# Kernel tuning notes

Measured on AMD Instinct MI355X. Metric: run time of the kernel, lower is better.

Reference implementation:

```python
import jax, jax.numpy as jnp
import numpy as np

I = 16    # nutrition_input_size
H = 128   # hidden_size
B = 64
S = 4096
MLP = 64


def setup_inputs() -> dict:
    key = jax.random.key(0)
    ks = jax.random.split(key, 16)
    sc = 0.05
    inp = {
        "nutrition_data": jax.random.normal(ks[0], (B, S, I), dtype=jnp.float32),
        # GRU layer 0 (input size I)
        "w_ih0": sc * jax.random.normal(ks[1], (3 * H, I), dtype=jnp.float32),
        "w_hh0": sc * jax.random.normal(ks[2], (3 * H, H), dtype=jnp.float32),
        "b_ih0": sc * jax.random.normal(ks[3], (3 * H,), dtype=jnp.float32),
        "b_hh0": sc * jax.random.normal(ks[4], (3 * H,), dtype=jnp.float32),
        # GRU layer 1 (input size H)
        "w_ih1": sc * jax.random.normal(ks[5], (3 * H, H), dtype=jnp.float32),
        "w_hh1": sc * jax.random.normal(ks[6], (3 * H, H), dtype=jnp.float32),
        "b_ih1": sc * jax.random.normal(ks[7], (3 * H,), dtype=jnp.float32),
        "b_hh1": sc * jax.random.normal(ks[8], (3 * H,), dtype=jnp.float32),
        # metabolism increment head: Linear(H+I, 64) -> ReLU -> Linear(64, 1)
        "w1": sc * jax.random.normal(ks[9], (MLP, H + I), dtype=jnp.float32),
        "b1": sc * jax.random.normal(ks[10], (MLP,), dtype=jnp.float32),
        "w2": sc * jax.random.normal(ks[11], (1, MLP), dtype=jnp.float32),
        "b2": sc * jax.random.normal(ks[12], (1,), dtype=jnp.float32),
        "initial_metabolism": jnp.float32(2.5),
    }
    return inp


def _gru_layer(x, w_ih, w_hh, b_ih, b_hh):
    # x: [B, S, D]; PyTorch GRU cell math, gate order (r, z, n).
    gi = jnp.einsum("bsd,gd->bsg", x, w_ih) + b_ih  # [B, S, 3H]
    h0 = jnp.zeros((x.shape[0], w_hh.shape[1]), dtype=x.dtype)

    def step(h, gi_t):
        gh = h @ w_hh.T + b_hh  # [B, 3H]
        i_r, i_z, i_n = jnp.split(gi_t, 3, axis=-1)
        h_r, h_z, h_n = jnp.split(gh, 3, axis=-1)
        r = jax.nn.sigmoid(i_r + h_r)
        z = jax.nn.sigmoid(i_z + h_z)
        n = jnp.tanh(i_n + r * h_n)
        h_new = (1.0 - z) * n + z * h
        return h_new, h_new

    _, hs = jax.lax.scan(step, h0, jnp.swapaxes(gi, 0, 1))  # hs: [S, B, H]
    return jnp.swapaxes(hs, 0, 1)  # [B, S, H]


def reference(nutrition_data, w_ih0, w_hh0, b_ih0, b_hh0,
              w_ih1, w_hh1, b_ih1, b_hh1,
              w1, b1, w2, b2, initial_metabolism):
    # 2-layer GRU (dropout is inactive in eval; identical math without it)
    h1 = _gru_layer(nutrition_data, w_ih0, w_hh0, b_ih0, b_hh0)
    gru_out = _gru_layer(h1, w_ih1, w_hh1, b_ih1, b_hh1)  # [B, S, H]

    # Per-timestep head is independent of recurrence: batch it over all t,
    # then replace the sequential additive accumulation with a cumsum.
    combined = jnp.concatenate([gru_out, nutrition_data], axis=-1)  # [B, S, H+I]
    hdn = jax.nn.relu(jnp.einsum("bsf,mf->bsm", combined, w1) + b1)
    inc = jnp.tanh(jnp.einsum("bsm,om->bso", hdn, w2) + b2) * 0.125  # [B, S, 1]
    out = initial_metabolism + jnp.cumsum(inc, axis=1)  # [B, S, 1]
    return out
```

## Files before the change

### kernel.cpp

```cpp
#include <hip/hip_runtime.h>
#include <cmath>

#define B 64
#define S 4096
#define NI 16
#define H 128
#define F 144
#define CH 16
#define NCH (S / CH)

typedef _Float16 h2   __attribute__((ext_vector_type(2)));
typedef _Float16 h4v  __attribute__((ext_vector_type(4)));
typedef _Float16 h8   __attribute__((ext_vector_type(8)));
typedef float    f4v  __attribute__((ext_vector_type(4)));
typedef unsigned long long u64;
typedef u64 u64x2 __attribute__((ext_vector_type(2)));

__device__ __forceinline__ float rcp_fast(float x) { return __builtin_amdgcn_rcpf(x); }
__device__ __forceinline__ float sigf(float x) {
    return rcp_fast(1.0f + __expf(-x));
}
__device__ __forceinline__ float tanh_fast(float x) {
    const float e = __expf(-2.0f * x);
    return fmaf(2.0f, rcp_fast(1.0f + e), -1.0f);
}
__device__ __forceinline__ float quad_reduce(float v) {
    int t1 = __builtin_amdgcn_mov_dpp(__float_as_int(v), 0xB1, 0xf, 0xf, true);
    v += __int_as_float(t1);
    int t2 = __builtin_amdgcn_mov_dpp(__float_as_int(v), 0x4E, 0xf, 0xf, true);
    v += __int_as_float(t2);
    return v;
}
__device__ __forceinline__ float pair_reduce(float v) {
    int t1 = __builtin_amdgcn_mov_dpp(__float_as_int(v), 0xB1, 0xf, 0xf, true);
    v += __int_as_float(t1);
    return v;
}
__device__ __forceinline__ h2 cvt2(float a, float b) {
    h2 r; r[0] = (_Float16)a; r[1] = (_Float16)b; return r;
}
__device__ __forceinline__ void cvt8(const float* p, h2* w) {
    const float4 f0 = ((const float4*)p)[0];
    const float4 f1 = ((const float4*)p)[1];
    w[0] = cvt2(f0.x, f0.y); w[1] = cvt2(f0.z, f0.w);
    w[2] = cvt2(f1.x, f1.y); w[3] = cvt2(f1.z, f1.w);
}
__device__ __forceinline__ h8 cvt8v(const float* p) {
    const float4 f0 = ((const float4*)p)[0];
    const float4 f1 = ((const float4*)p)[1];
    h8 r;
    r[0] = (_Float16)f0.x; r[1] = (_Float16)f0.y;
    r[2] = (_Float16)f0.z; r[3] = (_Float16)f0.w;
    r[4] = (_Float16)f1.x; r[5] = (_Float16)f1.y;
    r[6] = (_Float16)f1.z; r[7] = (_Float16)f1.w;
    return r;
}
__device__ __forceinline__ void pin_h2(h2& v) {
    int t = __builtin_bit_cast(int, v);
    asm volatile("" : "+v"(t));
    v = __builtin_bit_cast(h2, t);
}
__device__ __forceinline__ void pin_f(float& v) {
    asm volatile("" : "+v"(v));
}
__device__ __forceinline__ void pin_h8(h8& v) {
    u64x2 t = __builtin_bit_cast(u64x2, v);
    u64 a = t[0], b = t[1];
    asm volatile("" : "+v"(a), "+v"(b));
    t[0] = a; t[1] = b;
    v = __builtin_bit_cast(h8, t);
}
__device__ __forceinline__ f4v mfma16(h8 a, h8 b, f4v c) {
    return __builtin_amdgcn_mfma_f32_16x16x32_f16(a, b, c, 0, 0, 0);
}

__device__ __forceinline__ void store_y0(void* p, uint2 v) {
    __hip_atomic_store((u64*)p, __builtin_bit_cast(u64, v),
                       __ATOMIC_RELAXED, __HIP_MEMORY_SCOPE_AGENT);
}
__device__ __forceinline__ h8 load_y0_h8(const _Float16* p) {
    u64x2 v;
    v[0] = __hip_atomic_load((const u64*)p,     __ATOMIC_RELAXED, __HIP_MEMORY_SCOPE_AGENT);
    v[1] = __hip_atomic_load((const u64*)p + 1, __ATOMIC_RELAXED, __HIP_MEMORY_SCOPE_AGENT);
    return __builtin_bit_cast(h8, v);
}
__device__ __forceinline__ void wait_flag(int* f) {
    int spins = 0;
    while (__hip_atomic_load(f, __ATOMIC_ACQUIRE, __HIP_MEMORY_SCOPE_AGENT) == 0) {
        __builtin_amdgcn_s_sleep(8);
        if (++spins > (1 << 17)) break;
    }
}
__device__ __forceinline__ void post_flag(int* f) {
    __hip_atomic_store(f, 1, __ATOMIC_RELEASE, __HIP_MEMORY_SCOPE_AGENT);
}

__global__ __launch_bounds__(512, 2)
void gru_pipe(const float* __restrict__ x,
              const float* __restrict__ w_ih0, const float* __restrict__ w_hh0,
              const float* __restrict__ b_ih0, const float* __restrict__ b_hh0,
              const float* __restrict__ w_ih1, const float* __restrict__ w_hh1,
              const float* __restrict__ b_ih1, const float* __restrict__ b_hh1,
              _Float16* __restrict__ hbuf, int* __restrict__ flags)
{
    const int tid = threadIdx.x;
    const int b = blockIdx.x >> 1;
    const bool producer = (blockIdx.x & 1) == 0;

    if (producer) {
        const int j = tid >> 2;
        const int m = tid & 3;

        __shared__ __align__(16) _Float16 sH0[2][H];
        __shared__ __align__(16) _Float16 sX[2][CH][NI];
        __shared__ __align__(16) _Float16 sYo[2][CH][H];

        h2 wh[48];
        h2 wx[6];
#pragma unroll
        for (int g = 0; g < 3; g++) {
            const float* wr = w_hh0 + (size_t)(g * H + j) * H;
#pragma unroll
            for (int i = 0; i < 4; i++) {
                const int f = (i + m) & 3;
                cvt8(wr + 32 * m + 8 * f, &wh[g * 16 + 4 * i]);
            }
            const float4 wv = *(const float4*)(w_ih0 + (size_t)(g * H + j) * NI + 4 * m);
            wx[g * 2 + 0] = cvt2(wv.x, wv.y);
            wx[g * 2 + 1] = cvt2(wv.z, wv.w);
        }
        float b_r  = b_ih0[j]       + b_hh0[j];
        float b_z  = b_ih0[H + j]   + b_hh0[H + j];
        float b_in = b_ih0[2*H + j];
        float b_hn = b_hh0[2*H + j];
#pragma unroll
        for (int i = 0; i < 48; i++) pin_h2(wh[i]);
#pragma unroll
        for (int i = 0; i < 6; i++) pin_h2(wx[i]);
        pin_f(b_r); pin_f(b_z); pin_f(b_in); pin_f(b_hn);

        const float* xb = x + (size_t)b * S * NI;
        _Float16*    yb = hbuf + (size_t)b * S * H;
        int*         fb = flags + b * NCH;

        float4 xreg = {0.f, 0.f, 0.f, 0.f};
        if (tid < H) sH0[0][tid] = (_Float16)0.0f;
        if (tid < 64) {
            const float4 v = ((const float4*)xb)[tid];
            h4v p; p[0] = (_Float16)v.x; p[1] = (_Float16)v.y;
                   p[2] = (_Float16)v.z; p[3] = (_Float16)v.w;
            ((h4v*)&sX[0][0][0])[tid] = p;
            xreg = ((const float4*)(xb + CH * NI))[tid];
        }
        float hprev = 0.0f;
        __syncthreads();

        for (int k = 0; k <= S; k++) {
            const int cur = k & 1;
            const int c0  = k >> 4;
            const int tw  = k & (CH - 1);

            if (tw == 0 && k >= CH) {
                const int cp = c0 - 1;
                const uint2 v = ((const uint2*)&sYo[cp & 1][0][0])[tid];
                store_y0((char*)(yb + (size_t)cp * CH * H) + 8 * tid, v);
            }
            if (tw == 1 && k >= CH + 1 && tid == 0) post_flag(fb + (c0 - 1));

            if (k < S) {
                if (tw == 0 && tid < 64) {
                    const int cn = c0 + 1;
                    if (cn < NCH) {
                        h4v p; p[0] = (_Float16)xreg.x; p[1] = (_Float16)xreg.y;
                               p[2] = (_Float16)xreg.z; p[3] = (_Float16)xreg.w;
                        ((h4v*)&sX[cn & 1][0][0])[tid] = p;
                        if (cn + 1 < NCH)
                            xreg = ((const float4*)(xb + (size_t)(cn + 1) * CH * NI))[tid];
                    }
                }

                const float4* hv = (const float4*)&sH0[cur][0];
                float ar = 0.f, az = 0.f, ahn = 0.f;
#pragma unroll
                for (int i = 0; i < 4; i++) {
                    const int f = (i + m) & 3;
                    const float4 q = hv[4 * m + f];
                    const h2 p0 = __builtin_bit_cast(h2, q.x);
                    const h2 p1 = __builtin_bit_cast(h2, q.y);
                    const h2 p2 = __builtin_bit_cast(h2, q.z);
                    const h2 p3 = __builtin_bit_cast(h2, q.w);
                    ar  = __builtin_amdgcn_fdot2(p0, wh[4*i+0],    ar,  false);
                    ar  = __builtin_amdgcn_fdot2(p1, wh[4*i+1],    ar,  false);
                    ar  = __builtin_amdgcn_fdot2(p2, wh[4*i+2],    ar,  false);
                    ar  = __builtin_amdgcn_fdot2(p3, wh[4*i+3],    ar,  false);
                    az  = __builtin_amdgcn_fdot2(p0, wh[16+4*i+0], az,  false);
                    az  = __builtin_amdgcn_fdot2(p1, wh[16+4*i+1], az,  false);
                    az  = __builtin_amdgcn_fdot2(p2, wh[16+4*i+2], az,  false);
                    az  = __builtin_amdgcn_fdot2(p3, wh[16+4*i+3], az,  false);
                    ahn = __builtin_amdgcn_fdot2(p0, wh[32+4*i+0], ahn, false);
                    ahn = __builtin_amdgcn_fdot2(p1, wh[32+4*i+1], ahn, false);
                    ahn = __builtin_amdgcn_fdot2(p2, wh[32+4*i+2], ahn, false);
                    ahn = __builtin_amdgcn_fdot2(p3, wh[32+4*i+3], ahn, false);
                }
                const float2 xq = *(const float2*)&sX[c0 & 1][tw][4 * m];
                const h2 x0 = __builtin_bit_cast(h2, xq.x);
                const h2 x1 = __builtin_bit_cast(h2, xq.y);
                float ain = 0.f;
                ar  = __builtin_amdgcn_fdot2(x0, wx[0], ar,  false);
                ar  = __builtin_amdgcn_fdot2(x1, wx[1], ar,  false);
                az  = __builtin_amdgcn_fdot2(x0, wx[2], az,  false);
                az  = __builtin_amdgcn_fdot2(x1, wx[3], az,  false);
                ain = __builtin_amdgcn_fdot2(x0, wx[4], ain, false);
                ain = __builtin_amdgcn_fdot2(x1, wx[5], ain, false);

                const float vr  = quad_reduce(ar)  + b_r;
                const float vz  = quad_reduce(az)  + b_z;
                const float vin = quad_reduce(ain) + b_in;
                const float vhn = quad_reduce(ahn) + b_hn;

                const float r  = sigf(vr);
                const float z  = sigf(vz);
                const float n  = tanh_fast(vin + r * vhn);
                const float hn = n + z * (hprev - n);
                hprev = hn;
                if (m == 0) {
                    sH0[cur ^ 1][j]     = (_Float16)hn;
                    sYo[c0 & 1][tw][j]  = (_Float16)hn;
                }
            }
            __syncthreads();
        }
        if (tid == 0) post_flag(fb + (NCH - 1));
    } else {
        __shared__ __align__(16) _Float16 sH1[2][H];
        __shared__ __align__(16) float    sGi[2][CH][3][H];
        __shared__ __align__(16) _Float16 sHo[2][CH][H];

        _Float16* yb = hbuf + (size_t)b * S * H;
        int*      fb = flags + b * NCH;

        const bool isRec = (tid < 256);
        const int lane = tid & 63;
        const int jr = (tid & 255) >> 1;
        const int mr = tid & 1;
        const int wv = (tid >> 6) - 4;
        const int nl = lane & 15;
        const int q  = lane >> 4;

        h2 wc[96];
        float b_hn = 0.0f;
        h8 Bf[6][4];
        float bias[6];
        h8 Apre[4];

        if (isRec) {
#pragma unroll
            for (int g = 0; g < 3; g++) {
#pragma unroll
                for (int i = 0; i < 8; i++) {
                    const int ii = (i + 4 * mr) & 7;
                    cvt8(w_hh1 + (size_t)(g * H + jr) * H + 64 * mr + 8 * ii,
                         &wc[g * 32 + 4 * i]);
                }
            }
            b_hn = b_hh1[2 * H + jr];
#pragma unroll
            for (int i = 0; i < 96; i++) pin_h2(wc[i]);
            pin_f(b_hn);
            if (tid < H) sH1[0][tid] = (_Float16)0.0f;
        } else {
#pragma unroll
            for (int tt = 0; tt < 6; tt++) {
                const int n = 16 * (wv * 6 + tt) + nl;
                const float* wr = w_ih1 + (size_t)n * H;
#pragma unroll
                for (int kc = 0; kc < 4; kc++)
                    Bf[tt][kc] = cvt8v(wr + 32 * kc + 8 * q);
                bias[tt] = b_ih1[n] + (n < 2 * H ? b_hh1[n] : 0.0f);
            }
#pragma unroll
            for (int tt = 0; tt < 6; tt++) {
#pragma unroll
                for (int kc = 0; kc < 4; kc++) pin_h8(Bf[tt][kc]);
                pin_f(bias[tt]);
            }
            if (lane == 0) wait_flag(fb + 0);
            {
                const _Float16* yrow = yb + (size_t)nl * H;
                h8 A0c[4];
#pragma unroll
                for (int kc = 0; kc < 4; kc++)
                    A0c[kc] = load_y0_h8(yrow + 32 * kc + 8 * q);
                f4v a0 = {0.f,0.f,0.f,0.f}, a1 = a0, a2 = a0, a3 = a0, a4 = a0, a5 = a0;
#pragma unroll
                for (int kc = 0; kc < 4; kc++) {
                    a0 = mfma16(A0c[kc], Bf[0][kc], a0);
                    a1 = mfma16(A0c[kc], Bf[1][kc], a1);
                    a2 = mfma16(A0c[kc], Bf[2][kc], a2);
                    a3 = mfma16(A0c[kc], Bf[3][kc], a3);
                    a4 = mfma16(A0c[kc], Bf[4][kc], a4);
                    a5 = mfma16(A0c[kc], Bf[5][kc], a5);
                }
                f4v accs[6] = {a0, a1, a2, a3, a4, a5};
                float* gp = &sGi[0][0][0][0];
#pragma unroll
                for (int tt = 0; tt < 6; tt++) {
                    const int n = 16 * (wv * 6 + tt) + nl;
                    const int g = n >> 7, jj = n & 127;
#pragma unroll
                    for (int r = 0; r < 4; r++)
                        gp[((4 * q + r) * 3 + g) * H + jj] = accs[tt][r] + bias[tt];
                }
            }
        }
        float hprev = 0.0f;
        __syncthreads();

        for (int t = 0; t < S; t++) {
            const int cur = t & 1;
            const int c   = t >> 4;
            const int tw  = t & (CH - 1);

            if (isRec) {
                const float gr = sGi[c & 1][tw][0][jr];
                const float gz = sGi[c & 1][tw][1][jr];
                const float gn = sGi[c & 1][tw][2][jr];
                const float4* hv = (const float4*)&sH1[cur][0];
                float ar = 0.f, az = 0.f, ahn = 0.f;
#pragma unroll
                for (int i = 0; i < 8; i++) {
                    const int ii = (i + 4 * mr) & 7;
                    const float4 qv = hv[8 * mr + ii];
                    const h2 p0 = __builtin_bit_cast(h2, qv.x);
                    const h2 p1 = __builtin_bit_cast(h2, qv.y);
                    const h2 p2 = __builtin_bit_cast(h2, qv.z);
                    const h2 p3 = __builtin_bit_cast(h2, qv.w);
                    ar  = __builtin_amdgcn_fdot2(p0, wc[4*i+0],      ar,  false);
                    ar  = __builtin_amdgcn_fdot2(p1, wc[4*i+1],      ar,  false);
                    ar  = __builtin_amdgcn_fdot2(p2, wc[4*i+2],      ar,  false);
                    ar  = __builtin_amdgcn_fdot2(p3, wc[4*i+3],      ar,  false);
                    az  = __builtin_amdgcn_fdot2(p0, wc[32+4*i+0],   az,  false);
                    az  = __builtin_amdgcn_fdot2(p1, wc[32+4*i+1],   az,  false);
                    az  = __builtin_amdgcn_fdot2(p2, wc[32+4*i+2],   az,  false);
                    az  = __builtin_amdgcn_fdot2(p3, wc[32+4*i+3],   az,  false);
                    ahn = __builtin_amdgcn_fdot2(p0, wc[64+4*i+0],   ahn, false);
                    ahn = __builtin_amdgcn_fdot2(p1, wc[64+4*i+1],   ahn, false);
                    ahn = __builtin_amdgcn_fdot2(p2, wc[64+4*i+2],   ahn, false);
                    ahn = __builtin_amdgcn_fdot2(p3, wc[64+4*i+3],   ahn, false);
                }
                const float r  = sigf(pair_reduce(ar) + gr);
                const float z  = sigf(pair_reduce(az) + gz);
                const float n  = tanh_fast(gn + r * (pair_reduce(ahn) + b_hn));
                const float hn = n + z * (hprev - n);
                hprev = hn;
                if (mr == 0) {
                    sH1[cur ^ 1][jr]   = (_Float16)hn;
                    sHo[c & 1][tw][jr] = (_Float16)hn;
                }
            } else {
                if (tw == 0) {
                    if (c >= 1) {
                        const int cp  = c - 1;
                        const int idx = tid - 256;
                        const uint2 v0 = ((const uint2*)&sHo[cp & 1][0][0])[idx];
                        const uint2 v1 = ((const uint2*)&sHo[cp & 1][0][0])[idx + 256];
                        ((uint2*)(yb + (size_t)cp * CH * H))[idx]       = v0;
                        ((uint2*)(yb + (size_t)cp * CH * H))[idx + 256] = v1;
                    }
                    if (c + 1 < NCH) {
                        if (lane == 0) wait_flag(fb + (c + 1));
                        const _Float16* yrow = yb + ((size_t)(c + 1) * CH + nl) * H;
#pragma unroll
                        for (int kc = 0; kc < 4; kc++)
                            Apre[kc] = load_y0_h8(yrow + 32 * kc + 8 * q);
                    }
                } else if (tw == 1 && c + 1 < NCH) {
                    f4v a0 = {0.f,0.f,0.f,0.f}, a1 = a0, a2 = a0, a3 = a0, a4 = a0, a5 = a0;
#pragma unroll
                    for (int kc = 0; kc < 4; kc++) {
                        a0 = mfma16(Apre[kc], Bf[0][kc], a0);
                        a1 = mfma16(Apre[kc], Bf[1][kc], a1);
                        a2 = mfma16(Apre[kc], Bf[2][kc], a2);
                        a3 = mfma16(Apre[kc], Bf[3][kc], a3);
                        a4 = mfma16(Apre[kc], Bf[4][kc], a4);
                        a5 = mfma16(Apre[kc], Bf[5][kc], a5);
                    }
                    f4v accs[6] = {a0, a1, a2, a3, a4, a5};
                    float* gp = &sGi[(c + 1) & 1][0][0][0];
#pragma unroll
                    for (int tt = 0; tt < 6; tt++) {
                        const int n = 16 * (wv * 6 + tt) + nl;
                        const int g = n >> 7, jj = n & 127;
#pragma unroll
                        for (int r = 0; r < 4; r++)
                            gp[((4 * q + r) * 3 + g) * H + jj] = accs[tt][r] + bias[tt];
                    }
                }
            }
            __syncthreads();
        }
        if (!isRec) {
            const int cp  = NCH - 1;
            const int idx = tid - 256;
            const uint2 v0 = ((const uint2*)&sHo[cp & 1][0][0])[idx];
            const uint2 v1 = ((const uint2*)&sHo[cp & 1][0][0])[idx + 256];
            ((uint2*)(yb + (size_t)cp * CH * H))[idx]       = v0;
            ((uint2*)(yb + (size_t)cp * CH * H))[idx + 256] = v1;
        }
    }
}

__global__ __launch_bounds__(256, 2)
void head_mfma(const _Float16* __restrict__ h1, const float* __restrict__ x,
               const float* __restrict__ w1, const float* __restrict__ b1,
               const float* __restrict__ w2, const float* __restrict__ b2,
               float* __restrict__ inc)
{
    const int wave = threadIdx.x >> 6;
    const int lane = threadIdx.x & 63;
    const int nl   = lane & 15;
    const int q    = lane >> 4;

    h8 Bf[4][5];
    float b1v[4], w2v[4];
#pragma unroll
    for (int t = 0; t < 4; t++) {
        const int n = 16 * t + nl;
        const float* wr = w1 + (size_t)n * F;
#pragma unroll
        for (int c = 0; c < 4; c++)
            Bf[t][c] = cvt8v(wr + 32 * c + 8 * q);
        if (q < 2) Bf[t][4] = cvt8v(wr + 128 + 8 * q);
        else { h8 z = {};
               Bf[t][4] = z; }
        b1v[t] = b1[n];
        w2v[t] = w2[n];
    }
    const float b2v = b2[0];

    const int gw = blockIdx.x * 4 + wave;

    for (int it = 0; it < 8; it++) {
        const int row0 = (gw * 8 + it) * 16;
        const int rm   = row0 + nl;

        const _Float16* hp = h1 + (size_t)rm * H;
        h8 A0 = *(const h8*)(hp + 8 * q);
        h8 A1 = *(const h8*)(hp + 32 + 8 * q);
        h8 A2 = *(const h8*)(hp + 64 + 8 * q);
        h8 A3 = *(const h8*)(hp + 96 + 8 * q);
        h8 A4;
        if (q < 2) A4 = cvt8v(x + (size_t)rm * NI + 8 * q);
        else { h8 z = {}; A4 = z; }

        f4v acc0 = {0.f,0.f,0.f,0.f}, acc1 = {0.f,0.f,0.f,0.f};
        f4v acc2 = {0.f,0.f,0.f,0.f}, acc3 = {0.f,0.f,0.f,0.f};
        acc0 = mfma16(A0, Bf[0][0], acc0); acc1 = mfma16(A0, Bf[1][0], acc1);
        acc2 = mfma16(A0, Bf[2][0], acc2); acc3 = mfma16(A0, Bf[3][0], acc3);
        acc0 = mfma16(A1, Bf[0][1], acc0); acc1 = mfma16(A1, Bf[1][1], acc1);
        acc2 = mfma16(A1, Bf[2][1], acc2); acc3 = mfma16(A1, Bf[3][1], acc3);
        acc0 = mfma16(A2, Bf[0][2], acc0); acc1 = mfma16(A2, Bf[1][2], acc1);
        acc2 = mfma16(A2, Bf[2][2], acc2); acc3 = mfma16(A2, Bf[3][2], acc3);
        acc0 = mfma16(A3, Bf[0][3], acc0); acc1 = mfma16(A3, Bf[1][3], acc1);
        acc2 = mfma16(A3, Bf[2][3], acc2); acc3 = mfma16(A3, Bf[3][3], acc3);
        acc0 = mfma16(A4, Bf[0][4], acc0); acc1 = mfma16(A4, Bf[1][4], acc1);
        acc2 = mfma16(A4, Bf[2][4], acc2); acc3 = mfma16(A4, Bf[3][4], acc3);

        float rs[4];
#pragma unroll
        for (int r = 0; r < 4; r++) {
            rs[r] = fmaxf(acc0[r] + b1v[0], 0.f) * w2v[0]
                  + fmaxf(acc1[r] + b1v[1], 0.f) * w2v[1]
                  + fmaxf(acc2[r] + b1v[2], 0.f) * w2v[2]
                  + fmaxf(acc3[r] + b1v[3], 0.f) * w2v[3];
        }
#pragma unroll
        for (int off = 1; off < 16; off <<= 1) {
#pragma unroll
            for (int r = 0; r < 4; r++)
                rs[r] += __shfl_xor(rs[r], off, 64);
        }
        if (nl == 0) {
            float4 o;
            o.x = tanh_fast(rs[0] + b2v) * 0.125f;
            o.y = tanh_fast(rs[1] + b2v) * 0.125f;
            o.z = tanh_fast(rs[2] + b2v) * 0.125f;
            o.w = tanh_fast(rs[3] + b2v) * 0.125f;
            *(float4*)(inc + row0 + 4 * q) = o;
        }
    }
}

__global__ __launch_bounds__(256)
void cumsum_kernel(const float* __restrict__ inc, const float* __restrict__ init,
                   float* __restrict__ out)
{
    __shared__ float sW[4];
    const int b = blockIdx.x;
    const int tid = threadIdx.x;
    const int lane = tid & 63;
    const int wid = tid >> 6;

    const float* ib = inc + (size_t)b * S;
    float v[16];
#pragma unroll
    for (int i = 0; i < 16; i++) v[i] = ib[tid * 16 + i];

    float run = 0.f;
#pragma unroll
    for (int i = 0; i < 16; i++) { run += v[i]; v[i] = run; }

    float t = run;
#pragma unroll
    for (int off = 1; off < 64; off <<= 1) {
        float u = __shfl_up(t, off, 64);
        if (lane >= off) t += u;
    }
    const float excl = t - run;
    if (lane == 63) sW[wid] = t;
    __syncthreads();

    float wo = 0.f;
#pragma unroll
    for (int w = 0; w < 4; w++) if (w < wid) wo += sW[w];

    const float prefix = wo + excl + init[0];
    float* ob = out + (size_t)b * S;
#pragma unroll
    for (int i = 0; i < 16; i++) ob[tid * 16 + i] = prefix + v[i];
}

extern "C" void kernel_launch(void* const* d_in, const int* in_sizes, int n_in,
                              void* d_out, int out_size, void* d_ws, size_t ws_size,
                              hipStream_t stream)
{
    (void)in_sizes; (void)n_in; (void)out_size; (void)ws_size;
    const float* x     = (const float*)d_in[0];
    const float* w_ih0 = (const float*)d_in[1];
    const float* w_hh0 = (const float*)d_in[2];
    const float* b_ih0 = (const float*)d_in[3];
    const float* b_hh0 = (const float*)d_in[4];
    const float* w_ih1 = (const float*)d_in[5];
    const float* w_hh1 = (const float*)d_in[6];
    const float* b_ih1 = (const float*)d_in[7];
    const float* b_hh1 = (const float*)d_in[8];
    const float* w1    = (const float*)d_in[9];
    const float* b1    = (const float*)d_in[10];
    const float* w2    = (const float*)d_in[11];
    const float* b2    = (const float*)d_in[12];
    const float* init  = (const float*)d_in[13];
    float* out = (float*)d_out;

    _Float16* hbuf = (_Float16*)d_ws;
    float* incbuf  = (float*)((char*)d_ws + (size_t)B * S * H * 2);
    int* flags     = (int*)((char*)d_ws + (size_t)B * S * H * 2
                                        + (size_t)B * S * 4);

    hipMemsetAsync(flags, 0, (size_t)B * NCH * sizeof(int), stream);

    hipLaunchKernelGGL(gru_pipe, dim3(2 * B), dim3(512), 0, stream,
                       x, w_ih0, w_hh0, b_ih0, b_hh0,
                       w_ih1, w_hh1, b_ih1, b_hh1, hbuf, flags);
    hipLaunchKernelGGL(head_mfma, dim3(512), dim3(256), 0, stream,
                       hbuf, x, w1, b1, w2, b2, incbuf);
    hipLaunchKernelGGL(cumsum_kernel, dim3(B), dim3(256), 0, stream,
                       incbuf, init, out);
}
```

Before: 2.511 ms.

## Unify producer and consumer GRU blocks with MFMA input projection for layer 0

```diff
diff --git a/kernel.cpp b/kernel.cpp
--- a/kernel.cpp
+++ b/kernel.cpp
@@ -8,9 +8,9 @@
 #define F 144
 #define CH 16
 #define NCH (S / CH)
+#define GIP 201
 
 typedef _Float16 h2   __attribute__((ext_vector_type(2)));
-typedef _Float16 h4v  __attribute__((ext_vector_type(4)));
 typedef _Float16 h8   __attribute__((ext_vector_type(8)));
 typedef float    f4v  __attribute__((ext_vector_type(4)));
 typedef unsigned long long u64;
@@ -23,13 +23,6 @@
 __device__ __forceinline__ float tanh_fast(float x) {
     const float e = __expf(-2.0f * x);
     return fmaf(2.0f, rcp_fast(1.0f + e), -1.0f);
-}
-__device__ __forceinline__ float quad_reduce(float v) {
-    int t1 = __builtin_amdgcn_mov_dpp(__float_as_int(v), 0xB1, 0xf, 0xf, true);
-    v += __int_as_float(t1);
-    int t2 = __builtin_amdgcn_mov_dpp(__float_as_int(v), 0x4E, 0xf, 0xf, true);
-    v += __int_as_float(t2);
-    return v;
 }
 __device__ __forceinline__ float pair_reduce(float v) {
     int t1 = __builtin_amdgcn_mov_dpp(__float_as_int(v), 0xB1, 0xf, 0xf, true);
@@ -95,7 +88,19 @@
     __hip_atomic_store(f, 1, __ATOMIC_RELEASE, __HIP_MEMORY_SCOPE_AGENT);
 }
 
-__global__ __launch_bounds__(512, 2)
+__device__ __forceinline__ void write_gi(float* gp, const f4v* accs,
+                                         const float* bias, int wv, int nl, int q) {
+#pragma unroll
+    for (int tt = 0; tt < 6; tt++) {
+        const int n = 16 * (wv * 6 + tt) + nl;
+        const int g = n >> 7, jj = n & 127;
+#pragma unroll
+        for (int r = 0; r < 4; r++)
+            gp[((4 * q + r) * 3 + g) * GIP + jj] = accs[tt][r] + bias[tt];
+    }
+}
+
+__global__ __launch_bounds__(512, 1)
 void gru_pipe(const float* __restrict__ x,
               const float* __restrict__ w_ih0, const float* __restrict__ w_hh0,
               const float* __restrict__ b_ih0, const float* __restrict__ b_hh0,
@@ -103,311 +108,204 @@
               const float* __restrict__ b_ih1, const float* __restrict__ b_hh1,
               _Float16* __restrict__ hbuf, int* __restrict__ flags)
 {
+    __shared__ __align__(16) _Float16 sH[2][H];
+    __shared__ __align__(16) float    sGi[2][CH][3][GIP];
+    __shared__ __align__(16) _Float16 sO[2][CH][H];
+
     const int tid = threadIdx.x;
     const int b = blockIdx.x >> 1;
     const bool producer = (blockIdx.x & 1) == 0;
-
-    if (producer) {
-        const int j = tid >> 2;
-        const int m = tid & 3;
-
-        __shared__ __align__(16) _Float16 sH0[2][H];
-        __shared__ __align__(16) _Float16 sX[2][CH][NI];
-        __shared__ __align__(16) _Float16 sYo[2][CH][H];
-
-        h2 wh[48];
-        h2 wx[6];
-#pragma unroll
-        for (int g = 0; g < 3; g++) {
-            const float* wr = w_hh0 + (size_t)(g * H + j) * H;
-#pragma unroll
-            for (int i = 0; i < 4; i++) {
-                const int f = (i + m) & 3;
-                cvt8(wr + 32 * m + 8 * f, &wh[g * 16 + 4 * i]);
+    const bool isRec = tid < 256;
+    const int lane = tid & 63;
+    const int jr = (tid & 255) >> 1;
+    const int mr = tid & 1;
+    const int wv = (tid >> 6) - 4;
+    const int nl = lane & 15;
+    const int q  = lane >> 4;
+
+    const float* xb = x + (size_t)b * S * NI;
+    _Float16*    yb = hbuf + (size_t)b * S * H;
+    int*         fb = flags + b * NCH;
+
+    h2 wc[96];
+    float b_hn = 0.0f;
+    h8 Bf[6][4];
+    float bias[6];
+    h8 Apre[4];
+
+    if (isRec) {
+        const float* whh = producer ? w_hh0 : w_hh1;
+        const float* bhh = producer ? b_hh0 : b_hh1;
+#pragma unroll
+        for (int g = 0; g < 3; g++)
+#pragma unroll
+            for (int i = 0; i < 8; i++) {
+                const int ii = (i + 4 * mr) & 7;
+                cvt8(whh + (size_t)(g * H + jr) * H + 64 * mr + 8 * ii,
+                     &wc[g * 32 + 4 * i]);
             }
-            const float4 wv = *(const float4*)(w_ih0 + (size_t)(g * H + j) * NI + 4 * m);
-            wx[g * 2 + 0] = cvt2(wv.x, wv.y);
-            wx[g * 2 + 1] = cvt2(wv.z, wv.w);
-        }
-        float b_r  = b_ih0[j]       + b_hh0[j];
-        float b_z  = b_ih0[H + j]   + b_hh0[H + j];
-        float b_in = b_ih0[2*H + j];
-        float b_hn = b_hh0[2*H + j];
-#pragma unroll
-        for (int i = 0; i < 48; i++) pin_h2(wh[i]);
-#pragma unroll
-        for (int i = 0; i < 6; i++) pin_h2(wx[i]);
-        pin_f(b_r); pin_f(b_z); pin_f(b_in); pin_f(b_hn);
-
-        const float* xb = x + (size_t)b * S * NI;
-        _Float16*    yb = hbuf + (size_t)b * S * H;
-        int*         fb = flags + b * NCH;
-
-        float4 xreg = {0.f, 0.f, 0.f, 0.f};
-        if (tid < H) sH0[0][tid] = (_Float16)0.0f;
-        if (tid < 64) {
-            const float4 v = ((const float4*)xb)[tid];
-            h4v p; p[0] = (_Float16)v.x; p[1] = (_Float16)v.y;
-                   p[2] = (_Float16)v.z; p[3] = (_Float16)v.w;
-            ((h4v*)&sX[0][0][0])[tid] = p;
-            xreg = ((const float4*)(xb + CH * NI))[tid];
-        }
-        float hprev = 0.0f;
-        __syncthreads();
-
-        for (int k = 0; k <= S; k++) {
-            const int cur = k & 1;
-            const int c0  = k >> 4;
-            const int tw  = k & (CH - 1);
-
-            if (tw == 0 && k >= CH) {
-                const int cp = c0 - 1;
-                const uint2 v = ((const uint2*)&sYo[cp & 1][0][0])[tid];
-                store_y0((char*)(yb + (size_t)cp * CH * H) + 8 * tid, v);
+        b_hn = bhh[2 * H + jr];
+#pragma unroll
+        for (int i = 0; i < 96; i++) pin_h2(wc[i]);
+        pin_f(b_hn);
+        if (tid < H) sH[0][tid] = (_Float16)0.0f;
+    } else if (producer) {
+#pragma unroll
+        for (int tt = 0; tt < 6; tt++) {
+            const int n = 16 * (wv * 6 + tt) + nl;
+            if (q < 2) Bf[tt][0] = cvt8v(w_ih0 + (size_t)n * NI + 8 * q);
+            else { h8 z = {}; Bf[tt][0] = z; }
+            bias[tt] = b_ih0[n] + (n < 2 * H ? b_hh0[n] : 0.0f);
+            pin_h8(Bf[tt][0]); pin_f(bias[tt]);
+        }
+        h8 A;
+        if (q < 2) A = cvt8v(xb + (size_t)nl * NI + 8 * q);
+        else { h8 z = {}; A = z; }
+        f4v accs[6];
+#pragma unroll
+        for (int tt = 0; tt < 6; tt++) {
+            f4v zz = {0.f, 0.f, 0.f, 0.f};
+            accs[tt] = mfma16(A, Bf[tt][0], zz);
+        }
+        write_gi(&sGi[0][0][0][0], accs, bias, wv, nl, q);
+    } else {
+#pragma unroll
+        for (int tt = 0; tt < 6; tt++) {
+            const int n = 16 * (wv * 6 + tt) + nl;
+            const float* wr = w_ih1 + (size_t)n * H;
+#pragma unroll
+            for (int kc = 0; kc < 4; kc++) {
+                Bf[tt][kc] = cvt8v(wr + 32 * kc + 8 * q);
+                pin_h8(Bf[tt][kc]);
             }
-            if (tw == 1 && k >= CH + 1 && tid == 0) post_flag(fb + (c0 - 1));
-
-            if (k < S) {
-                if (tw == 0 && tid < 64) {
-                    const int cn = c0 + 1;
-                    if (cn < NCH) {
-                        h4v p; p[0] = (_Float16)xreg.x; p[1] = (_Float16)xreg.y;
-                               p[2] = (_Float16)xreg.z; p[3] = (_Float16)xreg.w;
-                        ((h4v*)&sX[cn & 1][0][0])[tid] = p;
-                        if (cn + 1 < NCH)
-                            xreg = ((const float4*)(xb + (size_t)(cn + 1) * CH * NI))[tid];
-                    }
-                }
-
-                const float4* hv = (const float4*)&sH0[cur][0];
-                float ar = 0.f, az = 0.f, ahn = 0.f;
-#pragma unroll
-                for (int i = 0; i < 4; i++) {
-                    const int f = (i + m) & 3;
-                    const float4 q = hv[4 * m + f];
-                    const h2 p0 = __builtin_bit_cast(h2, q.x);
-                    const h2 p1 = __builtin_bit_cast(h2, q.y);
-                    const h2 p2 = __builtin_bit_cast(h2, q.z);
-                    const h2 p3 = __builtin_bit_cast(h2, q.w);
-                    ar  = __builtin_amdgcn_fdot2(p0, wh[4*i+0],    ar,  false);
-                    ar  = __builtin_amdgcn_fdot2(p1, wh[4*i+1],    ar,  false);
-                    ar  = __builtin_amdgcn_fdot2(p2, wh[4*i+2],    ar,  false);
-                    ar  = __builtin_amdgcn_fdot2(p3, wh[4*i+3],    ar,  false);
-                    az  = __builtin_amdgcn_fdot2(p0, wh[16+4*i+0], az,  false);
-                    az  = __builtin_amdgcn_fdot2(p1, wh[16+4*i+1], az,  false);
-                    az  = __builtin_amdgcn_fdot2(p2, wh[16+4*i+2], az,  false);
-                    az  = __builtin_amdgcn_fdot2(p3, wh[16+4*i+3], az,  false);
-                    ahn = __builtin_amdgcn_fdot2(p0, wh[32+4*i+0], ahn, false);
-                    ahn = __builtin_amdgcn_fdot2(p1, wh[32+4*i+1], ahn, false);
-                    ahn = __builtin_amdgcn_fdot2(p2, wh[32+4*i+2], ahn, false);
-                    ahn = __builtin_amdgcn_fdot2(p3, wh[32+4*i+3], ahn, false);
-                }
-                const float2 xq = *(const float2*)&sX[c0 & 1][tw][4 * m];
-                const h2 x0 = __builtin_bit_cast(h2, xq.x);
-                const h2 x1 = __builtin_bit_cast(h2, xq.y);
-                float ain = 0.f;
-                ar  = __builtin_amdgcn_fdot2(x0, wx[0], ar,  false);
-                ar  = __builtin_amdgcn_fdot2(x1, wx[1], ar,  false);
-                az  = __builtin_amdgcn_fdot2(x0, wx[2], az,  false);
-                az  = __builtin_amdgcn_fdot2(x1, wx[3], az,  false);
-                ain = __builtin_amdgcn_fdot2(x0, wx[4], ain, false);
-                ain = __builtin_amdgcn_fdot2(x1, wx[5], ain, false);
-
-                const float vr  = quad_reduce(ar)  + b_r;
-                const float vz  = quad_reduce(az)  + b_z;
-                const float vin = quad_reduce(ain) + b_in;
-                const float vhn = quad_reduce(ahn) + b_hn;
-
-                const float r  = sigf(vr);
-                const float z  = sigf(vz);
-                const float n  = tanh_fast(vin + r * vhn);
-                const float hn = n + z * (hprev - n);
-                hprev = hn;
-                if (m == 0) {
-                    sH0[cur ^ 1][j]     = (_Float16)hn;
-                    sYo[c0 & 1][tw][j]  = (_Float16)hn;
-                }
+            bias[tt] = b_ih1[n] + (n < 2 * H ? b_hh1[n] : 0.0f);
+            pin_f(bias[tt]);
+        }
+        if (lane == 0) wait_flag(fb + 0);
+        const _Float16* yrow = yb + (size_t)nl * H;
+        h8 A0c[4];
+#pragma unroll
+        for (int kc = 0; kc < 4; kc++)
+            A0c[kc] = load_y0_h8(yrow + 32 * kc + 8 * q);
+        f4v accs[6];
+#pragma unroll
+        for (int tt = 0; tt < 6; tt++) { f4v zz = {0.f,0.f,0.f,0.f}; accs[tt] = zz; }
+#pragma unroll
+        for (int kc = 0; kc < 4; kc++)
+#pragma unroll
+            for (int tt = 0; tt < 6; tt++)
+                accs[tt] = mfma16(A0c[kc], Bf[tt][kc], accs[tt]);
+        write_gi(&sGi[0][0][0][0], accs, bias, wv, nl, q);
+    }
+    float hprev = 0.0f;
+    __syncthreads();
+
+    for (int t = 0; t < S; t++) {
+        const int cur = t & 1;
+        const int c   = t >> 4;
+        const int tw  = t & (CH - 1);
+
+        if (isRec) {
+            const float gr = sGi[c & 1][tw][0][jr];
+            const float gz = sGi[c & 1][tw][1][jr];
+            const float gn = sGi[c & 1][tw][2][jr];
+            const float4* hv = (const float4*)&sH[cur][0];
+            float ar = 0.f, az = 0.f, ahn = 0.f;
+#pragma unroll
+            for (int i = 0; i < 8; i++) {
+                const int ii = (i + 4 * mr) & 7;
+                const float4 qv = hv[8 * mr + ii];
+                const h2 p0 = __builtin_bit_cast(h2, qv.x);
+                const h2 p1 = __builtin_bit_cast(h2, qv.y);
+                const h2 p2 = __builtin_bit_cast(h2, qv.z);
+                const h2 p3 = __builtin_bit_cast(h2, qv.w);
+                ar  = __builtin_amdgcn_fdot2(p0, wc[4*i+0],    ar,  false);
+                ar  = __builtin_amdgcn_fdot2(p1, wc[4*i+1],    ar,  false);
+                ar  = __builtin_amdgcn_fdot2(p2, wc[4*i+2],    ar,  false);
+                ar  = __builtin_amdgcn_fdot2(p3, wc[4*i+3],    ar,  false);
+                az  = __builtin_amdgcn_fdot2(p0, wc[32+4*i+0], az,  false);
+                az  = __builtin_amdgcn_fdot2(p1, wc[32+4*i+1], az,  false);
+                az  = __builtin_amdgcn_fdot2(p2, wc[32+4*i+2], az,  false);
+                az  = __builtin_amdgcn_fdot2(p3, wc[32+4*i+3], az,  false);
+                ahn = __builtin_amdgcn_fdot2(p0, wc[64+4*i+0], ahn, false);
+                ahn = __builtin_amdgcn_fdot2(p1, wc[64+4*i+1], ahn, false);
+                ahn = __builtin_amdgcn_fdot2(p2, wc[64+4*i+2], ahn, false);
+                ahn = __builtin_amdgcn_fdot2(p3, wc[64+4*i+3], ahn, false);
             }
-            __syncthreads();
-        }
-        if (tid == 0) post_flag(fb + (NCH - 1));
-    } else {
-        __shared__ __align__(16) _Float16 sH1[2][H];
-        __shared__ __align__(16) float    sGi[2][CH][3][H];
-        __shared__ __align__(16) _Float16 sHo[2][CH][H];
-
-        _Float16* yb = hbuf + (size_t)b * S * H;
-        int*      fb = flags + b * NCH;
-
-        const bool isRec = (tid < 256);
-        const int lane = tid & 63;
-        const int jr = (tid & 255) >> 1;
-        const int mr = tid & 1;
-        const int wv = (tid >> 6) - 4;
-        const int nl = lane & 15;
-        const int q  = lane >> 4;
-
-        h2 wc[96];
-        float b_hn = 0.0f;
-        h8 Bf[6][4];
-        float bias[6];
-        h8 Apre[4];
-
-        if (isRec) {
-#pragma unroll
-            for (int g = 0; g < 3; g++) {
-#pragma unroll
-                for (int i = 0; i < 8; i++) {
-                    const int ii = (i + 4 * mr) & 7;
-                    cvt8(w_hh1 + (size_t)(g * H + jr) * H + 64 * mr + 8 * ii,
-                         &wc[g * 32 + 4 * i]);
-                }
+            const float r  = sigf(pair_reduce(ar) + gr);
+            const float z  = sigf(pair_reduce(az) + gz);
+            const float n  = tanh_fast(gn + r * (pair_reduce(ahn) + b_hn));
+            const float hn = n + z * (hprev - n);
+            hprev = hn;
+            if (mr == 0) {
+                sH[cur ^ 1][jr]   = (_Float16)hn;
+                sO[c & 1][tw][jr] = (_Float16)hn;
             }
-            b_hn = b_hh1[2 * H + jr];
-#pragma unroll
-            for (int i = 0; i < 96; i++) pin_h2(wc[i]);
-            pin_f(b_hn);
-            if (tid < H) sH1[0][tid] = (_Float16)0.0f;
         } else {
-#pragma unroll
-            for (int tt = 0; tt < 6; tt++) {
-                const int n = 16 * (wv * 6 + tt) + nl;
-                const float* wr = w_ih1 + (size_t)n * H;
-#pragma unroll
-                for (int kc = 0; kc < 4; kc++)
-                    Bf[tt][kc] = cvt8v(wr + 32 * kc + 8 * q);
-                bias[tt] = b_ih1[n] + (n < 2 * H ? b_hh1[n] : 0.0f);
-            }
-#pragma unroll
-            for (int tt = 0; tt < 6; tt++) {
-#pragma unroll
-                for (int kc = 0; kc < 4; kc++) pin_h8(Bf[tt][kc]);
-                pin_f(bias[tt]);
-            }
-            if (lane == 0) wait_flag(fb + 0);
-            {
-                const _Float16* yrow = yb + (size_t)nl * H;
-                h8 A0c[4];
-#pragma unroll
-                for (int kc = 0; kc < 4; kc++)
-                    A0c[kc] = load_y0_h8(yrow + 32 * kc + 8 * q);
-                f4v a0 = {0.f,0.f,0.f,0.f}, a1 = a0, a2 = a0, a3 = a0, a4 = a0, a5 = a0;
-#pragma unroll
-                for (int kc = 0; kc < 4; kc++) {
-                    a0 = mfma16(A0c[kc], Bf[0][kc], a0);
-                    a1 = mfma16(A0c[kc], Bf[1][kc], a1);
-                    a2 = mfma16(A0c[kc], Bf[2][kc], a2);
-                    a3 = mfma16(A0c[kc], Bf[3][kc], a3);
-                    a4 = mfma16(A0c[kc], Bf[4][kc], a4);
-                    a5 = mfma16(A0c[kc], Bf[5][kc], a5);
-                }
-                f4v accs[6] = {a0, a1, a2, a3, a4, a5};
-                float* gp = &sGi[0][0][0][0];
-#pragma unroll
-                for (int tt = 0; tt < 6; tt++) {
-                    const int n = 16 * (wv * 6 + tt) + nl;
-                    const int g = n >> 7, jj = n & 127;
-#pragma unroll
-                    for (int r = 0; r < 4; r++)
-                        gp[((4 * q + r) * 3 + g) * H + jj] = accs[tt][r] + bias[tt];
-                }
-            }
-        }
-        float hprev = 0.0f;
-        __syncthreads();
-
-        for (int t = 0; t < S; t++) {
-            const int cur = t & 1;
-            const int c   = t >> 4;
-            const int tw  = t & (CH - 1);
-
-            if (isRec) {
-                const float gr = sGi[c & 1][tw][0][jr];
-                const float gz = sGi[c & 1][tw][1][jr];
-                const float gn = sGi[c & 1][tw][2][jr];
-                const float4* hv = (const float4*)&sH1[cur][0];
-                float ar = 0.f, az = 0.f, ahn = 0.f;
-#pragma unroll
-                for (int i = 0; i < 8; i++) {
-                    const int ii = (i + 4 * mr) & 7;
-                    const float4 qv = hv[8 * mr + ii];
-                    const h2 p0 = __builtin_bit_cast(h2, qv.x);
-                    const h2 p1 = __builtin_bit_cast(h2, qv.y);
-                    const h2 p2 = __builtin_bit_cast(h2, qv.z);
-                    const h2 p3 = __builtin_bit_cast(h2, qv.w);
-                    ar  = __builtin_amdgcn_fdot2(p0, wc[4*i+0],      ar,  false);
-                    ar  = __builtin_amdgcn_fdot2(p1, wc[4*i+1],      ar,  false);
-                    ar  = __builtin_amdgcn_fdot2(p2, wc[4*i+2],      ar,  false);
-                    ar  = __builtin_amdgcn_fdot2(p3, wc[4*i+3],      ar,  false);
-                    az  = __builtin_amdgcn_fdot2(p0, wc[32+4*i+0],   az,  false);
-                    az  = __builtin_amdgcn_fdot2(p1, wc[32+4*i+1],   az,  false);
-                    az  = __builtin_amdgcn_fdot2(p2, wc[32+4*i+2],   az,  false);
-                    az  = __builtin_amdgcn_fdot2(p3, wc[32+4*i+3],   az,  false);
-                    ahn = __builtin_amdgcn_fdot2(p0, wc[64+4*i+0],   ahn, false);
-                    ahn = __builtin_amdgcn_fdot2(p1, wc[64+4*i+1],   ahn, false);
-                    ahn = __builtin_amdgcn_fdot2(p2, wc[64+4*i+2],   ahn, false);
-                    ahn = __builtin_amdgcn_fdot2(p3, wc[64+4*i+3],   ahn, false);
-                }
-                const float r  = sigf(pair_reduce(ar) + gr);
-                const float z  = sigf(pair_reduce(az) + gz);
-                const float n  = tanh_fast(gn + r * (pair_reduce(ahn) + b_hn));
-                const float hn = n + z * (hprev - n);
-                hprev = hn;
-                if (mr == 0) {
-                    sH1[cur ^ 1][jr]   = (_Float16)hn;
-                    sHo[c & 1][tw][jr] = (_Float16)hn;
-                }
-            } else {
-                if (tw == 0) {
-                    if (c >= 1) {
-                        const int cp  = c - 1;
-                        const int idx = tid - 256;
-                        const uint2 v0 = ((const uint2*)&sHo[cp & 1][0][0])[idx];
-                        const uint2 v1 = ((const uint2*)&sHo[cp & 1][0][0])[idx + 256];
+            if (tw == 0) {
+                if (c >= 1) {
+                    const int cp  = c - 1;
+                    const int idx = tid - 256;
+                    const uint2 v0 = ((const uint2*)&sO[cp & 1][0][0])[idx];
+                    const uint2 v1 = ((const uint2*)&sO[cp & 1][0][0])[idx + 256];
+                    if (producer) {
+                        store_y0((char*)(yb + (size_t)cp * CH * H) + 8 * idx, v0);
+                        store_y0((char*)(yb + (size_t)cp * CH * H) + 8 * (idx + 256), v1);
+                    } else {
                         ((uint2*)(yb + (size_t)cp * CH * H))[idx]       = v0;
                         ((uint2*)(yb + (size_t)cp * CH * H))[idx + 256] = v1;
                     }
-                    if (c + 1 < NCH) {
+                }
+                if (c + 1 < NCH) {
+                    if (producer) {
+                        if (q < 2) Apre[0] = cvt8v(xb + ((size_t)(c + 1) * CH + nl) * NI + 8 * q);
+                        else { h8 z = {}; Apre[0] = z; }
+                    } else {
                         if (lane == 0) wait_flag(fb + (c + 1));
-                        const _Float16* yrow = yb + ((size_t)(c + 1) * CH + nl) * H;
+                        const _Float16* yr2 = yb + ((size_t)(c + 1) * CH + nl) * H;
 #pragma unroll
                         for (int kc = 0; kc < 4; kc++)
-                            Apre[kc] = load_y0_h8(yrow + 32 * kc + 8 * q);
-                    }
-                } else if (tw == 1 && c + 1 < NCH) {
-                    f4v a0 = {0.f,0.f,0.f,0.f}, a1 = a0, a2 = a0, a3 = a0, a4 = a0, a5 = a0;
-#pragma unroll
-                    for (int kc = 0; kc < 4; kc++) {
-                        a0 = mfma16(Apre[kc], Bf[0][kc], a0);
-                        a1 = mfma16(Apre[kc], Bf[1][kc], a1);
-                        a2 = mfma16(Apre[kc], Bf[2][kc], a2);
-                        a3 = mfma16(Apre[kc], Bf[3][kc], a3);
-                        a4 = mfma16(Apre[kc], Bf[4][kc], a4);
-                        a5 = mfma16(Apre[kc], Bf[5][kc], a5);
-                    }
-                    f4v accs[6] = {a0, a1, a2, a3, a4, a5};
-                    float* gp = &sGi[(c + 1) & 1][0][0][0];
-#pragma unroll
-                    for (int tt = 0; tt < 6; tt++) {
-                        const int n = 16 * (wv * 6 + tt) + nl;
-                        const int g = n >> 7, jj = n & 127;
-#pragma unroll
-                        for (int r = 0; r < 4; r++)
-                            gp[((4 * q + r) * 3 + g) * H + jj] = accs[tt][r] + bias[tt];
+                            Apre[kc] = load_y0_h8(yr2 + 32 * kc + 8 * q);
                     }
                 }
+            } else if (tw == 1) {
+                if (producer && c >= 1 && tid == 256) post_flag(fb + (c - 1));
+                if (c + 1 < NCH) {
+                    f4v accs[6];
+#pragma unroll
+                    for (int tt = 0; tt < 6; tt++) { f4v zz = {0.f,0.f,0.f,0.f}; accs[tt] = zz; }
+                    if (producer) {
+#pragma unroll
+                        for (int tt = 0; tt < 6; tt++)
+                            accs[tt] = mfma16(Apre[0], Bf[tt][0], accs[tt]);
+                    } else {
+#pragma unroll
+                        for (int kc = 0; kc < 4; kc++)
+#pragma unroll
+                            for (int tt = 0; tt < 6; tt++)
+                                accs[tt] = mfma16(Apre[kc], Bf[tt][kc], accs[tt]);
+                    }
+                    write_gi(&sGi[(c + 1) & 1][0][0][0], accs, bias, wv, nl, q);
+                }
             }
-            __syncthreads();
-        }
-        if (!isRec) {
-            const int cp  = NCH - 1;
-            const int idx = tid - 256;
-            const uint2 v0 = ((const uint2*)&sHo[cp & 1][0][0])[idx];
-            const uint2 v1 = ((const uint2*)&sHo[cp & 1][0][0])[idx + 256];
+        }
+        __syncthreads();
+    }
+    if (!isRec) {
+        const int cp  = NCH - 1;
+        const int idx = tid - 256;
+        const uint2 v0 = ((const uint2*)&sO[cp & 1][0][0])[idx];
+        const uint2 v1 = ((const uint2*)&sO[cp & 1][0][0])[idx + 256];
+        if (producer) {
+            store_y0((char*)(yb + (size_t)cp * CH * H) + 8 * idx, v0);
+            store_y0((char*)(yb + (size_t)cp * CH * H) + 8 * (idx + 256), v1);
+        } else {
             ((uint2*)(yb + (size_t)cp * CH * H))[idx]       = v0;
             ((uint2*)(yb + (size_t)cp * CH * H))[idx + 256] = v1;
         }
     }
+    __syncthreads();
+    if (producer && tid == 256) post_flag(fb + (NCH - 1));
 }
 
 __global__ __launch_bounds__(256, 2)
```

Result: slower. 3.078 ms (+22.6%).
